# Kernel tuning notes

Hardware: AMD Instinct MI355X
Metric: run time of the kernel (lower is better)

## Reference

```python
import jax, jax.numpy as jnp
import numpy as np

DS = 8  # downsample_factor


def learned_upflow(flow, mask, ds=DS):
    """Convex-combination upsampling, faithful to Model.learned_upflow.

    flow: (n, 2, h, w)   coarse flow at 1/ds resolution
    mask: (n, 9*ds*ds, h, w)  raw (pre-softmax) convex weights
    returns: (n, 2, ds*h, ds*w)
    """
    n, _, h, w = flow.shape
    # mask.view(n, 1, 9, ds, ds, h, w); softmax over the 9 neighbor taps
    m = mask.reshape(n, 1, 9, ds, ds, h, w)
    m = jax.nn.softmax(m, axis=2)

    # F.unfold(ds*flow, [3,3], padding=1) -> 3x3 neighborhoods, row-major
    # kernel order (dy outer, dx inner), channel-major — matches the
    # subsequent view(n, 2, 9, 1, 1, h, w).
    fp = jnp.pad(ds * flow, ((0, 0), (0, 0), (1, 1), (1, 1)))
    patches = jnp.stack(
        [fp[:, :, dy:dy + h, dx:dx + w] for dy in range(3) for dx in range(3)],
        axis=2,
    )  # (n, 2, 9, h, w)

    up = jnp.sum(m * patches[:, :, :, None, None, :, :], axis=2)  # (n,2,ds,ds,h,w)
    # permute(0,1,4,2,5,3) then reshape -> (n, 2, ds*h, ds*w)
    up = up.transpose(0, 1, 4, 2, 5, 3)
    return up.reshape(n, 2, ds * h, ds * w)


def setup_inputs() -> dict:
    key = jax.random.key(0)
    k1, k2 = jax.random.split(key)
    n, h, w = 4, 136, 240
    flow = jax.random.normal(k1, (n, 2, h, w), dtype=jnp.float32)
    mask = jax.random.normal(k2, (n, 9 * DS * DS, h, w), dtype=jnp.float32)
    return {"flow": flow, "mask": mask}


def reference(flow, mask):
    return learned_upflow(flow, mask)
```

## Files before the change

kernel.cpp:

```cpp
#include <hip/hip_runtime.h>

#define HH 136
#define WW 240
#define HW (HH * WW)
#define DS 8
#define OW (DS * WW)
#define OH (DS * HH)
#define CROWS 8
#define NCH 9
#define NBUF 3

typedef float vf4 __attribute__((ext_vector_type(4)));

__device__ __forceinline__ void gload_lds16(const float* g, float* l) {
  __builtin_amdgcn_global_load_lds(
      (const __attribute__((address_space(1))) void*)g,
      (__attribute__((address_space(3))) void*)l, 16, 0, 0);
}

__global__ __launch_bounds__(256, 7) void upflow_kernel(
    const float* __restrict__ flow,
    const float* __restrict__ mask,
    float* __restrict__ out) {
  __shared__ float lm[NBUF][CROWS][WW];

  int h = blockIdx.x;
  int ni = blockIdx.y;
  int i = ni & 7;
  int n = ni >> 3;
  int tid = threadIdx.x;
  int w = tid >> 6, lane = tid & 63;
  int px = tid;

  float f0[9], f1[9];
  if (px < WW) {
    const float* fb0 = flow + (size_t)(n * 2 + 0) * HW;
    const float* fb1 = flow + (size_t)(n * 2 + 1) * HW;
#pragma unroll
    for (int dy = 0; dy < 3; ++dy) {
      int hh = h + dy - 1;
      bool rok = (hh >= 0) && (hh < HH);
#pragma unroll
      for (int dx = 0; dx < 3; ++dx) {
        int k = dy * 3 + dx;
        int cc = px + dx - 1;
        bool ok = rok && (cc >= 0) && (cc < WW);
        int idx = hh * WW + cc;
        f0[k] = ok ? 8.0f * fb0[idx] : 0.0f;
        f1[k] = ok ? 8.0f * fb1[idx] : 0.0f;
      }
    }
  }

  const float* mrow = mask + ((size_t)n * 576 + i * 8) * HW + (size_t)h * WW;

  if (lane < 60) {
#pragma unroll
    for (int t = 0; t < 2; ++t) {
      int j = 2 * w + t;
      gload_lds16(mrow + (size_t)(0 * 64 + j) * HW + lane * 4, &lm[0][j][0]);
    }
#pragma unroll
    for (int t = 0; t < 2; ++t) {
      int j = 2 * w + t;
      gload_lds16(mrow + (size_t)(1 * 64 + j) * HW + lane * 4, &lm[1][j][0]);
    }
  }

  const float L2E = 1.4426950408889634f;
  float sj[8], d0j[8], d1j[8];
#pragma unroll
  for (int j = 0; j < 8; ++j) { sj[j] = 0.f; d0j[j] = 0.f; d1j[j] = 0.f; }

#pragma unroll
  for (int c = 0; c < NCH; ++c) {
    if (c + 2 < NCH) {
      if (lane < 60) {
#pragma unroll
        for (int t = 0; t < 2; ++t) {
          int j = 2 * w + t;
          gload_lds16(mrow + (size_t)((c + 2) * 64 + j) * HW + lane * 4,
                      &lm[(c + 2) % NBUF][j][0]);
        }
      }
      asm volatile("s_waitcnt vmcnt(4)" ::: "memory");
    } else if (c + 2 == NCH) {
      asm volatile("s_waitcnt vmcnt(2)" ::: "memory");
    } else {
      asm volatile("s_waitcnt vmcnt(0)" ::: "memory");
    }
    __builtin_amdgcn_s_barrier();
    asm volatile("" ::: "memory");

    if (px < WW) {
      const float fc0 = f0[c], fc1 = f1[c];
#pragma unroll
      for (int j = 0; j < 8; ++j) {
        float e = exp2f(lm[c % NBUF][j][px] * L2E);
        sj[j] += e;
        d0j[j] += e * fc0;
        d1j[j] += e * fc1;
      }
    }

    if (c + 1 < NCH) {
      asm volatile("" ::: "memory");
      __builtin_amdgcn_s_barrier();
      asm volatile("" ::: "memory");
    }
  }

  if (px < WW) {
    size_t ob0 =
        ((size_t)(n * 2 + 0) * OH + (size_t)(h * 8 + i)) * (size_t)OW + px * 8;
    size_t ob1 = ob0 + (size_t)OH * OW;
    float r0 = 1.0f / sj[0], r1 = 1.0f / sj[1], r2 = 1.0f / sj[2],
          r3 = 1.0f / sj[3], r4 = 1.0f / sj[4], r5 = 1.0f / sj[5],
          r6 = 1.0f / sj[6], r7 = 1.0f / sj[7];
    vf4 a = {d0j[0] * r0, d0j[1] * r1, d0j[2] * r2, d0j[3] * r3};
    vf4 b = {d0j[4] * r4, d0j[5] * r5, d0j[6] * r6, d0j[7] * r7};
    vf4 c = {d1j[0] * r0, d1j[1] * r1, d1j[2] * r2, d1j[3] * r3};
    vf4 d = {d1j[4] * r4, d1j[5] * r5, d1j[6] * r6, d1j[7] * r7};
    *(vf4*)(out + ob0) = a;
    *(vf4*)(out + ob0 + 4) = b;
    *(vf4*)(out + ob1) = c;
    *(vf4*)(out + ob1 + 4) = d;
  }
}

extern "C" void kernel_launch(void* const* d_in, const int* in_sizes, int n_in,
                              void* d_out, int out_size, void* d_ws, size_t ws_size,
                              hipStream_t stream) {
  const float* flow = (const float*)d_in[0];
  const float* mask = (const float*)d_in[1];
  float* out = (float*)d_out;
  dim3 grid(HH, 32);
  upflow_kernel<<<grid, 256, 0, stream>>>(flow, mask, out);
}
```

Before: 75.67 us.

## Process two coarse rows per 512-thread block with double-buffered mask loads

Each block now handles two adjacent coarse rows with 512 threads, so 480 of them are active instead of 240 of 256. The number of blocks is halved. The mask pipeline drops from triple to double buffering, with one prefetch stage ahead. Each wave now loads both rows of one mask channel, giving contiguous 2-row chunks. This aims to waste fewer lanes and cut per-block overhead, at the cost of a shallower prefetch depth and lower block-level occupancy.

```diff
diff --git a/kernel.cpp b/kernel.cpp
--- a/kernel.cpp
+++ b/kernel.cpp
@@ -6,9 +6,8 @@
 #define DS 8
 #define OW (DS * WW)
 #define OH (DS * HH)
-#define CROWS 8
 #define NCH 9
-#define NBUF 3
+#define NBUF 2
 
 typedef float vf4 __attribute__((ext_vector_type(4)));
 
@@ -18,22 +17,33 @@
       (__attribute__((address_space(3))) void*)l, 16, 0, 0);
 }
 
-__global__ __launch_bounds__(256, 7) void upflow_kernel(
+__global__ __launch_bounds__(512, 4) void upflow_kernel(
     const float* __restrict__ flow,
     const float* __restrict__ mask,
     float* __restrict__ out) {
-  __shared__ float lm[NBUF][CROWS][WW];
+  __shared__ float lm[NBUF][8][2][WW];
 
-  int h = blockIdx.x;
+  int h0 = blockIdx.x * 2;
   int ni = blockIdx.y;
   int i = ni & 7;
   int n = ni >> 3;
   int tid = threadIdx.x;
   int w = tid >> 6, lane = tid & 63;
-  int px = tid;
+  int ph = tid / 240;
+  int px = tid - ph * 240;
+  bool act = tid < 480;
+  int h = h0 + ph;
+
+  const float* mrow = mask + ((size_t)n * 576 + i * 8) * HW + (size_t)h0 * WW;
+
+  if (lane < 60) {
+    const float* b = mrow + (size_t)w * HW;
+    gload_lds16(b + lane * 4, &lm[0][w][0][0]);
+    gload_lds16(b + WW + lane * 4, &lm[0][w][1][0]);
+  }
 
   float f0[9], f1[9];
-  if (px < WW) {
+  if (act) {
     const float* fb0 = flow + (size_t)(n * 2 + 0) * HW;
     const float* fb1 = flow + (size_t)(n * 2 + 1) * HW;
 #pragma unroll
@@ -52,21 +62,6 @@
     }
   }
 
-  const float* mrow = mask + ((size_t)n * 576 + i * 8) * HW + (size_t)h * WW;
-
-  if (lane < 60) {
-#pragma unroll
-    for (int t = 0; t < 2; ++t) {
-      int j = 2 * w + t;
-      gload_lds16(mrow + (size_t)(0 * 64 + j) * HW + lane * 4, &lm[0][j][0]);
-    }
-#pragma unroll
-    for (int t = 0; t < 2; ++t) {
-      int j = 2 * w + t;
-      gload_lds16(mrow + (size_t)(1 * 64 + j) * HW + lane * 4, &lm[1][j][0]);
-    }
-  }
-
   const float L2E = 1.4426950408889634f;
   float sj[8], d0j[8], d1j[8];
 #pragma unroll
@@ -74,17 +69,12 @@
 
 #pragma unroll
   for (int c = 0; c < NCH; ++c) {
-    if (c + 2 < NCH) {
+    if (c + 1 < NCH) {
       if (lane < 60) {
-#pragma unroll
-        for (int t = 0; t < 2; ++t) {
-          int j = 2 * w + t;
-          gload_lds16(mrow + (size_t)((c + 2) * 64 + j) * HW + lane * 4,
-                      &lm[(c + 2) % NBUF][j][0]);
-        }
+        const float* b = mrow + (size_t)((c + 1) * 64 + w) * HW;
+        gload_lds16(b + lane * 4, &lm[(c + 1) & 1][w][0][0]);
+        gload_lds16(b + WW + lane * 4, &lm[(c + 1) & 1][w][1][0]);
       }
-      asm volatile("s_waitcnt vmcnt(4)" ::: "memory");
-    } else if (c + 2 == NCH) {
       asm volatile("s_waitcnt vmcnt(2)" ::: "memory");
     } else {
       asm volatile("s_waitcnt vmcnt(0)" ::: "memory");
@@ -92,11 +82,11 @@
     __builtin_amdgcn_s_barrier();
     asm volatile("" ::: "memory");
 
-    if (px < WW) {
+    if (act) {
       const float fc0 = f0[c], fc1 = f1[c];
 #pragma unroll
       for (int j = 0; j < 8; ++j) {
-        float e = exp2f(lm[c % NBUF][j][px] * L2E);
+        float e = exp2f(lm[c & 1][j][ph][px] * L2E);
         sj[j] += e;
         d0j[j] += e * fc0;
         d1j[j] += e * fc1;
@@ -110,7 +100,7 @@
     }
   }
 
-  if (px < WW) {
+  if (act) {
     size_t ob0 =
         ((size_t)(n * 2 + 0) * OH + (size_t)(h * 8 + i)) * (size_t)OW + px * 8;
     size_t ob1 = ob0 + (size_t)OH * OW;
@@ -134,6 +124,6 @@
   const float* flow = (const float*)d_in[0];
   const float* mask = (const float*)d_in[1];
   float* out = (float*)d_out;
-  dim3 grid(HH, 32);
-  upflow_kernel<<<grid, 256, 0, stream>>>(flow, mask, out);
+  dim3 grid(HH / 2, 32);
+  upflow_kernel<<<grid, 512, 0, stream>>>(flow, mask, out);
 }
```

Measured after the change: 79.72 us. +5.3%, slower.
